# Performance work log

Measured on AMD Instinct MI355X. Metric: run time of the kernel, lower is better.

## Reference

```python
import jax, jax.numpy as jnp
import numpy as np

DX = 1.0  # voxel_spacing

def _grad(t, axis):
    """Central difference along `axis` with replicate (Neumann) boundaries.
    Matches F.pad(mode='replicate') + conv3d with a +/-0.5 stencil."""
    pad = [(0, 0)] * t.ndim
    pad[axis] = (1, 1)
    p = jnp.pad(t, pad, mode='edge')
    n = p.shape[axis]
    fwd = jax.lax.slice_in_dim(p, 2, n, axis=axis)
    bwd = jax.lax.slice_in_dim(p, 0, n - 2, axis=axis)
    return (fwd - bwd) * (0.5 / DX)

# axis mapping for [B, C, D, H, W]: grad_x -> W (4), grad_y -> H (3), grad_z -> D (2)
_AXES = (4, 3, 2)

def setup_inputs() -> dict:
    key = jax.random.key(0)
    k1, k2, k3 = jax.random.split(key, 3)
    shape = (4, 1, 192, 192, 192)
    u = jax.random.uniform(k1, shape, dtype=jnp.float32)
    D = jax.random.uniform(k2, shape, dtype=jnp.float32)
    rho = jax.random.uniform(k3, shape, dtype=jnp.float32)
    return {"u": u, "D": D, "rho": rho}

def reference(u, D, rho):
    # div(D * grad(u))
    div = jnp.zeros_like(u)
    for ax in _AXES:
        flux = D * _grad(u, ax)
        div = div + _grad(flux, ax)
    # du/dt = div(D grad u) + rho * u * (1 - u)
    return div + rho * u * (1.0 - u)
```

## Files before the change

### kernel.cpp

```cpp
#include <hip/hip_runtime.h>


#define NX   192
#define SP   (NX * NX)
#define TX   64
#define TY   16
#define ZC   24
#define LROW 68
#define SLAB (20 * LROW)

#define LD2(p, o) (*(const float2*)((p) + (o)))

__global__ __launch_bounds__(512, 4)
void fk_kernel(const float* __restrict__ u,
               const float* __restrict__ Dd,
               const float* __restrict__ rho,
               float* __restrict__ out)
{
    __shared__ float Ush[5 * SLAB];
    __shared__ float Dsh[3 * SLAB];

    const int tx  = threadIdx.x;
    const int ty  = threadIdx.y;
    const int tid = ty * 32 + tx;

    int bid = blockIdx.x;
    const int xt = bid % 3;  bid /= 3;
    const int yt = bid % 12; bid /= 12;
    const int zc = bid % 8;  bid /= 8;
    const int b  = bid;

    const int x0 = xt * TX, y0 = yt * TY, z0 = zc * ZC;

    const size_t vol = (size_t)b * NX * SP;
    const float* ub = u   + vol;
    const float* db = Dd  + vol;
    const float* rb = rho + vol;
    float*       ob = out + vol;

    int g0, g1, g2;
    {
        #pragma unroll
        for (int k = 0; k < 3; ++k) {
            const int p = tid + 512 * k;
            const int pp = (p < SLAB) ? p : 0;
            const int r = pp / LROW, c = pp % LROW;
            int gy = y0 + r - 2; gy = gy < 0 ? 0 : (gy > NX - 1 ? NX - 1 : gy);
            int gx = x0 + c - 2; gx = gx < 0 ? 0 : (gx > NX - 1 ? NX - 1 : gx);
            const int go = gy * NX + gx;
            if (k == 0) g0 = go; else if (k == 1) g1 = go; else g2 = go;
        }
    }
    const bool a2 = (tid < SLAB - 1024);

    #pragma unroll
    for (int s = 0; s < 5; ++s) {
        int pz = z0 - 2 + s; pz = pz < 0 ? 0 : pz;
        const float* src = ub + (size_t)pz * SP;
        Ush[s * SLAB + tid]       = src[g0];
        Ush[s * SLAB + tid + 512] = src[g1];
        if (a2) Ush[s * SLAB + tid + 1024] = src[g2];
    }
    #pragma unroll
    for (int s = 0; s < 3; ++s) {
        int pz = z0 - 1 + s; pz = pz < 0 ? 0 : pz;
        const float* src = db + (size_t)pz * SP;
        Dsh[s * SLAB + tid]       = src[g0];
        Dsh[s * SLAB + tid + 512] = src[g1];
        if (a2) Dsh[s * SLAB + tid + 1024] = src[g2];
    }
    __syncthreads();

    int su0 = 0, su1 = 1, su2 = 2, su3 = 3, su4 = 4;
    int sd0 = 0, sd1 = 1, sd2 = 2;

    const int x  = x0 + 2 * tx;
    const int y  = y0 + ty;
    const int bl = (ty + 2) * LROW + (2 * tx + 2);
    const size_t gcen = (size_t)y * NX + x;

    const bool fx0 = (x == 0);
    const bool fx1 = (x + 1 == NX - 1);
    const bool fy0 = (y == 0);
    const bool fy1 = (y == NX - 1);

    for (int iz = 0; iz < ZC; ++iz) {
        const int z = z0 + iz;
        const bool pf = (iz + 1 < ZC);

        float pu0, pu1, pu2, pd0, pd1, pd2;
        if (pf) {
            const int zu = (z + 3 > NX - 1) ? NX - 1 : z + 3;
            const int zd = (z + 2 > NX - 1) ? NX - 1 : z + 2;
            const float* us = ub + (size_t)zu * SP;
            const float* ds = db + (size_t)zd * SP;
            pu0 = us[g0]; pu1 = us[g1]; if (a2) pu2 = us[g2];
            pd0 = ds[g0]; pd1 = ds[g1]; if (a2) pd2 = ds[g2];
        }
        const float2 rc = *(const float2*)(rb + (size_t)z * SP + gcen);

        const float* Uc = Ush + su2 * SLAB;
        const float* Dc = Dsh + sd1 * SLAB;
        const float2 uc   = LD2(Uc, bl);
        const float2 uxm  = LD2(Uc, bl - 2);
        const float2 uxp  = LD2(Uc, bl + 2);
        const float2 uym  = LD2(Uc, bl - 2 * LROW);
        const float2 uyp  = LD2(Uc, bl + 2 * LROW);
        const float2 dc   = LD2(Dc, bl);
        const float2 dxm  = LD2(Dc, bl - 2);
        const float2 dxp  = LD2(Dc, bl + 2);
        const float2 dym  = LD2(Dc, bl - LROW);
        const float2 dyp  = LD2(Dc, bl + LROW);
        const float2 uzm2 = LD2(Ush + su0 * SLAB, bl);
        const float2 uzp2 = LD2(Ush + su4 * SLAB, bl);
        const float2 dzm  = LD2(Dsh + sd0 * SLAB, bl);
        const float2 dzp  = LD2(Dsh + sd2 * SLAB, bl);

        float divx_x = dc.y  * (uxp.x - uc.x) - dxm.y * (uc.x - uxm.x);
        float divx_y = dxp.x * (uxp.y - uc.y) - dc.x  * (uc.y - uxm.y);
        if (fx0) divx_x = dc.y * (uxp.x - uc.x) - dc.x * (uc.y - uc.x);
        if (fx1) divx_y = dc.y * (uc.y - uc.x)  - dc.x * (uc.y - uxm.y);

        float divy_x = dyp.x * (uyp.x - uc.x) - dym.x * (uc.x - uym.x);
        float divy_y = dyp.y * (uyp.y - uc.y) - dym.y * (uc.y - uym.y);
        if (fy0) {
            const float2 uyp1 = LD2(Uc, bl + LROW);
            divy_x = dyp.x * (uyp.x - uc.x) - dym.x * (uyp1.x - uc.x);
            divy_y = dyp.y * (uyp.y - uc.y) - dym.y * (uyp1.y - uc.y);
        }
        if (fy1) {
            const float2 uym1 = LD2(Uc, bl - LROW);
            divy_x = dyp.x * (uc.x - uym1.x) - dym.x * (uc.x - uym.x);
            divy_y = dyp.y * (uc.y - uym1.y) - dym.y * (uc.y - uym.y);
        }

        float divz_x = dzp.x * (uzp2.x - uc.x) - dzm.x * (uc.x - uzm2.x);
        float divz_y = dzp.y * (uzp2.y - uc.y) - dzm.y * (uc.y - uzm2.y);
        if (z == 0) {
            const float2 uzp1 = LD2(Ush + su3 * SLAB, bl);
            divz_x = dzp.x * (uzp2.x - uc.x) - dzm.x * (uzp1.x - uc.x);
            divz_y = dzp.y * (uzp2.y - uc.y) - dzm.y * (uzp1.y - uc.y);
        }
        if (z == NX - 1) {
            const float2 uzm1 = LD2(Ush + su1 * SLAB, bl);
            divz_x = dzp.x * (uc.x - uzm1.x) - dzm.x * (uc.x - uzm2.x);
            divz_y = dzp.y * (uc.y - uzm1.y) - dzm.y * (uc.y - uzm2.y);
        }

        float2 o;
        o.x = 0.25f * (divx_x + divy_x + divz_x) + rc.x * uc.x * (1.0f - uc.x);
        o.y = 0.25f * (divx_y + divy_y + divz_y) + rc.y * uc.y * (1.0f - uc.y);
        *(float2*)(ob + (size_t)z * SP + gcen) = o;

        __syncthreads();
        if (pf) {
            float* Uw = Ush + su0 * SLAB;
            float* Dw = Dsh + sd0 * SLAB;
            Uw[tid] = pu0; Uw[tid + 512] = pu1; if (a2) Uw[tid + 1024] = pu2;
            Dw[tid] = pd0; Dw[tid + 512] = pd1; if (a2) Dw[tid + 1024] = pd2;
            int t = su0; su0 = su1; su1 = su2; su2 = su3; su3 = su4; su4 = t;
            t = sd0; sd0 = sd1; sd1 = sd2; sd2 = t;
        }
        __syncthreads();
    }
}

extern "C" void kernel_launch(void* const* d_in, const int* in_sizes, int n_in,
                              void* d_out, int out_size, void* d_ws, size_t ws_size,
                              hipStream_t stream) {
    const float* u   = (const float*)d_in[0];
    const float* Dd  = (const float*)d_in[1];
    const float* rho = (const float*)d_in[2];
    float* out = (float*)d_out;

    dim3 block(32, 16, 1);
    const int grid = 3 * 12 * 8 * 4;
    fk_kernel<<<grid, block, 0, stream>>>(u, Dd, rho, out);
}
```

Measured before the change: 110.8 us.

## Add spare shared-memory slab to drop a barrier and retile to 48-wide blocks

Adds an extra U and D slab to the shared-memory ring buffer so the prefetched plane is written into a free slot, which removes one of the two __syncthreads per z-step. Also prefetches rho for the next plane a step ahead. Retiles blocks to 48x16 with 384 threads and doubles the z-chunk length to 48, trading less z-halo reloading for fewer blocks (768 instead of 1152) and more shared memory per block.

New measurement: 139.9 us. 1.26x slower.

```diff
diff --git a/kernel.cpp b/kernel.cpp
--- a/kernel.cpp
+++ b/kernel.cpp
@@ -3,34 +3,34 @@
 
 #define NX   192
 #define SP   (NX * NX)
-#define TX   64
-#define TY   16
-#define ZC   24
-#define LROW 68
-#define SLAB (20 * LROW)
+#define ZC   48
+#define LROW 52
+#define SROW 20
+#define SLAB (SROW * LROW)
+#define NTHR 384
 
 #define LD2(p, o) (*(const float2*)((p) + (o)))
 
-__global__ __launch_bounds__(512, 4)
+__global__ __launch_bounds__(NTHR, 4)
 void fk_kernel(const float* __restrict__ u,
                const float* __restrict__ Dd,
                const float* __restrict__ rho,
                float* __restrict__ out)
 {
-    __shared__ float Ush[5 * SLAB];
-    __shared__ float Dsh[3 * SLAB];
+    __shared__ float Ush[6 * SLAB];
+    __shared__ float Dsh[4 * SLAB];
 
     const int tx  = threadIdx.x;
     const int ty  = threadIdx.y;
-    const int tid = ty * 32 + tx;
+    const int tid = ty * 24 + tx;
 
     int bid = blockIdx.x;
-    const int xt = bid % 3;  bid /= 3;
+    const int xt = bid % 4;  bid /= 4;
     const int yt = bid % 12; bid /= 12;
-    const int zc = bid % 8;  bid /= 8;
+    const int zc = bid % 4;  bid /= 4;
     const int b  = bid;
 
-    const int x0 = xt * TX, y0 = yt * TY, z0 = zc * ZC;
+    const int x0 = xt * 48, y0 = yt * 16, z0 = zc * ZC;
 
     const size_t vol = (size_t)b * NX * SP;
     const float* ub = u   + vol;
@@ -42,7 +42,7 @@
     {
         #pragma unroll
         for (int k = 0; k < 3; ++k) {
-            const int p = tid + 512 * k;
+            const int p  = tid + NTHR * k;
             const int pp = (p < SLAB) ? p : 0;
             const int r = pp / LROW, c = pp % LROW;
             int gy = y0 + r - 2; gy = gy < 0 ? 0 : (gy > NX - 1 ? NX - 1 : gy);
@@ -51,28 +51,24 @@
             if (k == 0) g0 = go; else if (k == 1) g1 = go; else g2 = go;
         }
     }
-    const bool a2 = (tid < SLAB - 1024);
+    const bool a2 = (tid < SLAB - 2 * NTHR);
 
     #pragma unroll
     for (int s = 0; s < 5; ++s) {
         int pz = z0 - 2 + s; pz = pz < 0 ? 0 : pz;
         const float* src = ub + (size_t)pz * SP;
-        Ush[s * SLAB + tid]       = src[g0];
-        Ush[s * SLAB + tid + 512] = src[g1];
-        if (a2) Ush[s * SLAB + tid + 1024] = src[g2];
+        Ush[s * SLAB + tid]        = src[g0];
+        Ush[s * SLAB + tid + NTHR] = src[g1];
+        if (a2) Ush[s * SLAB + tid + 2 * NTHR] = src[g2];
     }
     #pragma unroll
     for (int s = 0; s < 3; ++s) {
         int pz = z0 - 1 + s; pz = pz < 0 ? 0 : pz;
         const float* src = db + (size_t)pz * SP;
-        Dsh[s * SLAB + tid]       = src[g0];
-        Dsh[s * SLAB + tid + 512] = src[g1];
-        if (a2) Dsh[s * SLAB + tid + 1024] = src[g2];
+        Dsh[s * SLAB + tid]        = src[g0];
+        Dsh[s * SLAB + tid + NTHR] = src[g1];
+        if (a2) Dsh[s * SLAB + tid + 2 * NTHR] = src[g2];
     }
-    __syncthreads();
-
-    int su0 = 0, su1 = 1, su2 = 2, su3 = 3, su4 = 4;
-    int sd0 = 0, sd1 = 1, sd2 = 2;
 
     const int x  = x0 + 2 * tx;
     const int y  = y0 + ty;
@@ -84,11 +80,18 @@
     const bool fy0 = (y == 0);
     const bool fy1 = (y == NX - 1);
 
+    float2 rcur = *(const float2*)(rb + (size_t)z0 * SP + gcen);
+    __syncthreads();
+
+    int su0 = 0, su1 = 1, su2 = 2, su3 = 3, su4 = 4, su5 = 5;
+    int sd0 = 0, sd1 = 1, sd2 = 2, sd3 = 3;
+
     for (int iz = 0; iz < ZC; ++iz) {
-        const int z = z0 + iz;
+        const int z  = z0 + iz;
         const bool pf = (iz + 1 < ZC);
 
         float pu0, pu1, pu2, pd0, pd1, pd2;
+        float2 rnx;
         if (pf) {
             const int zu = (z + 3 > NX - 1) ? NX - 1 : z + 3;
             const int zd = (z + 2 > NX - 1) ? NX - 1 : z + 2;
@@ -96,8 +99,8 @@
             const float* ds = db + (size_t)zd * SP;
             pu0 = us[g0]; pu1 = us[g1]; if (a2) pu2 = us[g2];
             pd0 = ds[g0]; pd1 = ds[g1]; if (a2) pd2 = ds[g2];
+            rnx = *(const float2*)(rb + (size_t)(z + 1) * SP + gcen);
         }
-        const float2 rc = *(const float2*)(rb + (size_t)z * SP + gcen);
 
         const float* Uc = Ush + su2 * SLAB;
         const float* Dc = Dsh + sd1 * SLAB;
@@ -148,20 +151,20 @@
         }
 
         float2 o;
-        o.x = 0.25f * (divx_x + divy_x + divz_x) + rc.x * uc.x * (1.0f - uc.x);
-        o.y = 0.25f * (divx_y + divy_y + divz_y) + rc.y * uc.y * (1.0f - uc.y);
+        o.x = 0.25f * (divx_x + divy_x + divz_x) + rcur.x * uc.x * (1.0f - uc.x);
+        o.y = 0.25f * (divx_y + divy_y + divz_y) + rcur.y * uc.y * (1.0f - uc.y);
         *(float2*)(ob + (size_t)z * SP + gcen) = o;
 
-        __syncthreads();
         if (pf) {
-            float* Uw = Ush + su0 * SLAB;
-            float* Dw = Dsh + sd0 * SLAB;
-            Uw[tid] = pu0; Uw[tid + 512] = pu1; if (a2) Uw[tid + 1024] = pu2;
-            Dw[tid] = pd0; Dw[tid + 512] = pd1; if (a2) Dw[tid + 1024] = pd2;
-            int t = su0; su0 = su1; su1 = su2; su2 = su3; su3 = su4; su4 = t;
-            t = sd0; sd0 = sd1; sd1 = sd2; sd2 = t;
+            float* Uw = Ush + su5 * SLAB;
+            float* Dw = Dsh + sd3 * SLAB;
+            Uw[tid] = pu0; Uw[tid + NTHR] = pu1; if (a2) Uw[tid + 2 * NTHR] = pu2;
+            Dw[tid] = pd0; Dw[tid + NTHR] = pd1; if (a2) Dw[tid + 2 * NTHR] = pd2;
+            __syncthreads();
+            int t = su0; su0 = su1; su1 = su2; su2 = su3; su3 = su4; su4 = su5; su5 = t;
+            t = sd0; sd0 = sd1; sd1 = sd2; sd2 = sd3; sd3 = t;
+            rcur = rnx;
         }
-        __syncthreads();
     }
 }
 
@@ -173,7 +176,7 @@
     const float* rho = (const float*)d_in[2];
     float* out = (float*)d_out;
 
-    dim3 block(32, 16, 1);
-    const int grid = 3 * 12 * 8 * 4;
+    dim3 block(24, 16, 1);
+    const int grid = 4 * 12 * 4 * 4;
     fk_kernel<<<grid, block, 0, stream>>>(u, Dd, rho, out);
 }
```
